# Optimization experiments

Hardware: AMD Instinct MI355X
Metric: run time of the kernel (lower is better)

## Reference

```python
import jax, jax.numpy as jnp
import numpy as np

STRIDE = 1
PADDING = 1
DILATION = 1


def setup_inputs() -> dict:
    key = jax.random.key(0)
    k1, k2 = jax.random.split(key)
    N, C_in, H, W = 32, 128, 56, 56
    C_out, ksz = 256, 3
    x = jax.random.normal(k1, (N, C_in, H, W), dtype=jnp.float32)
    # xavier_normal_ with gain sqrt(2): std = gain*sqrt(2/(fan_in+fan_out))
    fan_in = C_in * ksz * ksz
    fan_out = C_out * ksz * ksz
    std = np.sqrt(2.0) * np.sqrt(2.0 / (fan_in + fan_out))
    weight = jax.random.normal(k2, (C_out, C_in, ksz, ksz), dtype=jnp.float32) * jnp.float32(std)
    bias = jnp.zeros((C_out,), dtype=jnp.float32)
    return {"x": x, "weight": weight, "bias": bias}


def reference(x, weight, bias):
    # Faithful to conv2d(X, K, stride, padding, dilation, bias):
    # unfold (im2col) + matmul + fold is mathematically a standard cross-correlation
    # conv; expressed here with the efficient lax primitive.
    y = jax.lax.conv_general_dilated(
        x, weight,
        window_strides=(STRIDE, STRIDE),
        padding=[(PADDING, PADDING), (PADDING, PADDING)],
        rhs_dilation=(DILATION, DILATION),
        dimension_numbers=("NCHW", "OIHW", "NCHW"),
    )
    return y + bias[None, :, None, None]
```

## Files before the change

kernel.cpp:

```cpp
#include <hip/hip_runtime.h>
#include <hip/hip_bf16.h>


#define CIN   128
#define HH    56
#define WW    56
#define COUT  256
#define HW    3136
#define NIMG  32
#define NP    (NIMG * HW)
#define XPW   58
#define XPIX  (XPW * XPW)
#define XPAD_BYTES (NIMG * XPIX * CIN * 2)
#define WT_OFF     XPAD_BYTES

typedef __bf16 bf16x8 __attribute__((ext_vector_type(8)));
typedef float  f32x4  __attribute__((ext_vector_type(4)));

#define GLD16(g, l) __builtin_amdgcn_global_load_lds( \
    (const __attribute__((address_space(1))) void*)(g), \
    (__attribute__((address_space(3))) void*)(l), 16, 0, 0)

__global__ __launch_bounds__(128) void prep_x(const float* __restrict__ x,
                                              __hip_bfloat16* __restrict__ xp) {
    const int b = blockIdx.x;
    const int n = b / HH;
    const int y = b - n * HH;
    const int ci = threadIdx.x;
    const float* src = x + ((size_t)(n * CIN + ci) * HW) + y * WW;
    __hip_bfloat16* dst = xp + ((size_t)(n * XPIX + (y + 1) * XPW + 1)) * CIN + ci;
    for (int xx = 0; xx < WW; ++xx)
        dst[(size_t)xx * CIN] = __float2bfloat16(src[xx]);
}

__global__ __launch_bounds__(256) void prep_w(const float* __restrict__ w,
                                              __hip_bfloat16* __restrict__ wt) {
    const int co = blockIdx.x * 2 + (threadIdx.x >> 7);
    const int ci = threadIdx.x & 127;
    const float* src = w + (size_t)(co * CIN + ci) * 9;
    #pragma unroll
    for (int t = 0; t < 9; ++t)
        wt[(size_t)t * (COUT * CIN) + co * CIN + ci] = __float2bfloat16(src[t]);
}

__global__ __launch_bounds__(256) void conv_main(
    const char* __restrict__ xpb,
    const char* __restrict__ wtb,
    const float* __restrict__ bias,
    float* __restrict__ out)
{
    __shared__ __align__(16) char Alds[16384];
    __shared__ __align__(16) char Blds[16384];

    const int tid  = threadIdx.x;
    const int l    = tid & 63;
    const int wv   = tid >> 6;
    const int wm   = wv & 1;
    const int wn   = wv >> 1;
    const int l15  = l & 15;
    const int quad = l >> 4;
    const int lr   = l >> 3;
    const int ls   = l & 7;
    const int sg   = ls ^ lr;

    const int bm = blockIdx.x & 1;
    const int bn = blockIdx.x >> 1;
    const int pbase  = bn * 128;
    const int cobase = bm * 128;

    unsigned aoff[4], boff[4];
    #pragma unroll
    for (int j = 0; j < 4; ++j) {
        const int rowl = (wv * 4 + j) * 8 + lr;
        aoff[j] = (unsigned)((cobase + rowl) * 256 + sg * 16);
        const int p   = pbase + rowl;
        const int n   = p / HW;
        const int rem = p - n * HW;
        const int y   = rem / WW;
        const int x   = rem - y * WW;
        boff[j] = (unsigned)((n * XPIX + y * XPW + x) * 256 + sg * 16);
    }

    f32x4 acc[4][4];
    #pragma unroll
    for (int i = 0; i < 4; ++i)
        #pragma unroll
        for (int j = 0; j < 4; ++j)
            acc[i][j] = (f32x4){0.f, 0.f, 0.f, 0.f};

    #pragma unroll
    for (int t = 0; t < 9; ++t) {
        const int r = t / 3;
        const int s = t - 3 * r;
        #pragma unroll
        for (int hf = 0; hf < 2; ++hf) {
            const unsigned wo = (unsigned)(t * 65536 + hf * 128);
            const unsigned bo = (unsigned)((r * XPW + s) * 256 + hf * 128);

            __syncthreads();
            #pragma unroll
            for (int j = 0; j < 4; ++j) {
                GLD16(wtb + wo + aoff[j], Alds + (wv * 4 + j) * 1024);
                GLD16(xpb + bo + boff[j], Blds + (wv * 4 + j) * 1024);
            }
            __syncthreads();

            #pragma unroll
            for (int kg = 0; kg < 2; ++kg) {
                bf16x8 af[4], bfr[4];
                #pragma unroll
                for (int mt = 0; mt < 4; ++mt) {
                    const int row  = wm * 64 + mt * 16 + l15;
                    const int segl = (kg * 4 + quad) ^ (row & 7);
                    af[mt] = *(const bf16x8*)(Alds + row * 128 + segl * 16);
                }
                #pragma unroll
                for (int nt = 0; nt < 4; ++nt) {
                    const int row  = wn * 64 + nt * 16 + l15;
                    const int segl = (kg * 4 + quad) ^ (row & 7);
                    bfr[nt] = *(const bf16x8*)(Blds + row * 128 + segl * 16);
                }
                #pragma unroll
                for (int mt = 0; mt < 4; ++mt)
                    #pragma unroll
                    for (int nt = 0; nt < 4; ++nt)
                        acc[mt][nt] = __builtin_amdgcn_mfma_f32_16x16x32_bf16(
                            af[mt], bfr[nt], acc[mt][nt], 0, 0, 0);
            }
        }
    }

    #pragma unroll
    for (int nt = 0; nt < 4; ++nt) {
        const int pp = pbase + wn * 64 + nt * 16 + l15;
        const int n2 = pp / HW;
        const int r2 = pp - n2 * HW;
        float* ob = out + (size_t)n2 * (COUT * HW) + r2;
        #pragma unroll
        for (int mt = 0; mt < 4; ++mt) {
            const int co = cobase + wm * 64 + mt * 16 + quad * 4;
            const float4 bv = *(const float4*)(bias + co);
            f32x4 a = acc[mt][nt];
            ob[(size_t)(co + 0) * HW] = a[0] + bv.x;
            ob[(size_t)(co + 1) * HW] = a[1] + bv.y;
            ob[(size_t)(co + 2) * HW] = a[2] + bv.z;
            ob[(size_t)(co + 3) * HW] = a[3] + bv.w;
        }
    }
}

extern "C" void kernel_launch(void* const* d_in, const int* in_sizes, int n_in,
                              void* d_out, int out_size, void* d_ws, size_t ws_size,
                              hipStream_t stream) {
    const float* x = (const float*)d_in[0];
    const float* w = (const float*)d_in[1];
    const float* b = (const float*)d_in[2];
    char* ws = (char*)d_ws;
    __hip_bfloat16* xp = (__hip_bfloat16*)ws;
    __hip_bfloat16* wt = (__hip_bfloat16*)(ws + WT_OFF);

    hipMemsetAsync(ws, 0, XPAD_BYTES, stream);
    prep_x<<<dim3(NIMG * HH), dim3(128), 0, stream>>>(x, xp);
    prep_w<<<dim3(128), dim3(256), 0, stream>>>(w, wt);
    conv_main<<<dim3((NP / 128) * 2), dim3(256), 0, stream>>>(
        (const char*)xp, (const char*)wt, b, (float*)d_out);
}
```

Before: 215.1 us.

## Coalesce input prep via LDS transpose, drop memset, use full-K tiles per tap

prep_x now reads rows with float4 loads, transposes them through LDS and writes coalesced 16-byte stores, and zeroes only the padding border itself, which removes the full-buffer memset. Rounding changes from round-to-nearest to truncation. The conv kernel loads the whole 128-channel K slice per tap in one stage, halving the barriers, with a 16-segment XOR swizzle. Blocks are reordered so groups of 8 pixel tiles share an output-channel half, which may help L2 reuse. LDS use doubles to 64KB, which may cut occupancy.

```diff
diff --git a/kernel.cpp b/kernel.cpp
--- a/kernel.cpp
+++ b/kernel.cpp
@@ -21,16 +21,48 @@
     (const __attribute__((address_space(1))) void*)(g), \
     (__attribute__((address_space(3))) void*)(l), 16, 0, 0)
 
+__device__ __forceinline__ unsigned pack_bf16(float a, float b) {
+    return (__float_as_uint(b) & 0xFFFF0000u) | (__float_as_uint(a) >> 16);
+}
+
 __global__ __launch_bounds__(128) void prep_x(const float* __restrict__ x,
                                               __hip_bfloat16* __restrict__ xp) {
-    const int b = blockIdx.x;
-    const int n = b / HH;
-    const int y = b - n * HH;
+    __shared__ unsigned short t[HH * CIN];
+    const int b  = blockIdx.x;
+    const int n  = b / HH;
+    const int y  = b - n * HH;
     const int ci = threadIdx.x;
+
     const float* src = x + ((size_t)(n * CIN + ci) * HW) + y * WW;
-    __hip_bfloat16* dst = xp + ((size_t)(n * XPIX + (y + 1) * XPW + 1)) * CIN + ci;
-    for (int xx = 0; xx < WW; ++xx)
-        dst[(size_t)xx * CIN] = __float2bfloat16(src[xx]);
+    #pragma unroll
+    for (int j = 0; j < 14; ++j) {
+        const float4 v = ((const float4*)src)[j];
+        t[(4 * j + 0) * CIN + ci] = (unsigned short)(__float_as_uint(v.x) >> 16);
+        t[(4 * j + 1) * CIN + ci] = (unsigned short)(__float_as_uint(v.y) >> 16);
+        t[(4 * j + 2) * CIN + ci] = (unsigned short)(__float_as_uint(v.z) >> 16);
+        t[(4 * j + 3) * CIN + ci] = (unsigned short)(__float_as_uint(v.w) >> 16);
+    }
+
+    const uint4 z = make_uint4(0, 0, 0, 0);
+    if (ci < 32) {
+        const int side = ci >> 4;
+        const int j    = ci & 15;
+        ((uint4*)(xp + ((size_t)n * XPIX + (y + 1) * XPW + side * 57) * CIN))[j] = z;
+    }
+    if (y == 0)
+        for (int j = ci; j < 928; j += 128)
+            ((uint4*)(xp + (size_t)n * XPIX * CIN))[j] = z;
+    if (y == HH - 1)
+        for (int j = ci; j < 928; j += 128)
+            ((uint4*)(xp + ((size_t)n * XPIX + 57 * XPW) * CIN))[j] = z;
+
+    __syncthreads();
+
+    uint4* dst = (uint4*)(xp + ((size_t)n * XPIX + (y + 1) * XPW + 1) * CIN);
+    const uint4* lsrc = (const uint4*)t;
+    #pragma unroll
+    for (int j = 0; j < 7; ++j)
+        dst[j * 128 + ci] = lsrc[j * 128 + ci];
 }
 
 __global__ __launch_bounds__(256) void prep_w(const float* __restrict__ w,
@@ -39,8 +71,8 @@
     const int ci = threadIdx.x & 127;
     const float* src = w + (size_t)(co * CIN + ci) * 9;
     #pragma unroll
-    for (int t = 0; t < 9; ++t)
-        wt[(size_t)t * (COUT * CIN) + co * CIN + ci] = __float2bfloat16(src[t]);
+    for (int tp = 0; tp < 9; ++tp)
+        wt[(size_t)tp * (COUT * CIN) + co * CIN + ci] = __float2bfloat16(src[tp]);
 }
 
 __global__ __launch_bounds__(256) void conv_main(
@@ -49,8 +81,8 @@
     const float* __restrict__ bias,
     float* __restrict__ out)
 {
-    __shared__ __align__(16) char Alds[16384];
-    __shared__ __align__(16) char Blds[16384];
+    __shared__ __align__(16) char Alds[32768];
+    __shared__ __align__(16) char Blds[32768];
 
     const int tid  = threadIdx.x;
     const int l    = tid & 63;
@@ -59,26 +91,26 @@
     const int wn   = wv >> 1;
     const int l15  = l & 15;
     const int quad = l >> 4;
-    const int lr   = l >> 3;
-    const int ls   = l & 7;
-    const int sg   = ls ^ lr;
 
-    const int bm = blockIdx.x & 1;
-    const int bn = blockIdx.x >> 1;
+    const int idx = blockIdx.x;
+    const int bm  = (idx >> 3) & 1;
+    const int bn  = (idx >> 4) * 8 + (idx & 7);
     const int pbase  = bn * 128;
     const int cobase = bm * 128;
 
-    unsigned aoff[4], boff[4];
+    unsigned aoff[8], boff[8];
     #pragma unroll
-    for (int j = 0; j < 4; ++j) {
-        const int rowl = (wv * 4 + j) * 8 + lr;
-        aoff[j] = (unsigned)((cobase + rowl) * 256 + sg * 16);
-        const int p   = pbase + rowl;
+    for (int j = 0; j < 8; ++j) {
+        const int c    = wv * 8 + j;
+        const int row  = 4 * c + (l >> 4);
+        const int gseg = (l & 15) ^ (row & 15);
+        aoff[j] = (unsigned)((cobase + row) * 256 + gseg * 16);
+        const int p   = pbase + row;
         const int n   = p / HW;
         const int rem = p - n * HW;
         const int y   = rem / WW;
         const int x   = rem - y * WW;
-        boff[j] = (unsigned)((n * XPIX + y * XPW + x) * 256 + sg * 16);
+        boff[j] = (unsigned)((n * XPIX + y * XPW + x) * 256 + gseg * 16);
     }
 
     f32x4 acc[4][4];
@@ -92,41 +124,39 @@
     for (int t = 0; t < 9; ++t) {
         const int r = t / 3;
         const int s = t - 3 * r;
+        const unsigned wo = (unsigned)(t * (COUT * CIN * 2));
+        const unsigned bo = (unsigned)((r * XPW + s) * 256);
+
+        __syncthreads();
         #pragma unroll
-        for (int hf = 0; hf < 2; ++hf) {
-            const unsigned wo = (unsigned)(t * 65536 + hf * 128);
-            const unsigned bo = (unsigned)((r * XPW + s) * 256 + hf * 128);
+        for (int j = 0; j < 8; ++j) {
+            const int c = wv * 8 + j;
+            GLD16(wtb + wo + aoff[j], Alds + c * 1024);
+            GLD16(xpb + bo + boff[j], Blds + c * 1024);
+        }
+        __syncthreads();
 
-            __syncthreads();
+        #pragma unroll
+        for (int kg = 0; kg < 4; ++kg) {
+            bf16x8 af[4], bfr[4];
             #pragma unroll
-            for (int j = 0; j < 4; ++j) {
-                GLD16(wtb + wo + aoff[j], Alds + (wv * 4 + j) * 1024);
-                GLD16(xpb + bo + boff[j], Blds + (wv * 4 + j) * 1024);
+            for (int mt = 0; mt < 4; ++mt) {
+                const int row  = wm * 64 + mt * 16 + l15;
+                const int segl = (kg * 4 + quad) ^ l15;
+                af[mt] = *(const bf16x8*)(Alds + row * 256 + segl * 16);
             }
-            __syncthreads();
-
             #pragma unroll
-            for (int kg = 0; kg < 2; ++kg) {
-                bf16x8 af[4], bfr[4];
+            for (int nt = 0; nt < 4; ++nt) {
+                const int row  = wn * 64 + nt * 16 + l15;
+                const int segl = (kg * 4 + quad) ^ l15;
+                bfr[nt] = *(const bf16x8*)(Blds + row * 256 + segl * 16);
+            }
+            #pragma unroll
+            for (int mt = 0; mt < 4; ++mt)
                 #pragma unroll
-                for (int mt = 0; mt < 4; ++mt) {
-                    const int row  = wm * 64 + mt * 16 + l15;
-                    const int segl = (kg * 4 + quad) ^ (row & 7);
-                    af[mt] = *(const bf16x8*)(Alds + row * 128 + segl * 16);
-                }
-                #pragma unroll
-                for (int nt = 0; nt < 4; ++nt) {
-                    const int row  = wn * 64 + nt * 16 + l15;
-                    const int segl = (kg * 4 + quad) ^ (row & 7);
-                    bfr[nt] = *(const bf16x8*)(Blds + row * 128 + segl * 16);
-                }
-                #pragma unroll
-                for (int mt = 0; mt < 4; ++mt)
-                    #pragma unroll
-                    for (int nt = 0; nt < 4; ++nt)
-                        acc[mt][nt] = __builtin_amdgcn_mfma_f32_16x16x32_bf16(
-                            af[mt], bfr[nt], acc[mt][nt], 0, 0, 0);
-            }
+                for (int nt = 0; nt < 4; ++nt)
+                    acc[mt][nt] = __builtin_amdgcn_mfma_f32_16x16x32_bf16(
+                        af[mt], bfr[nt], acc[mt][nt], 0, 0, 0);
         }
     }
 
@@ -159,7 +189,6 @@
     __hip_bfloat16* xp = (__hip_bfloat16*)ws;
     __hip_bfloat16* wt = (__hip_bfloat16*)(ws + WT_OFF);
 
-    hipMemsetAsync(ws, 0, XPAD_BYTES, stream);
     prep_x<<<dim3(NIMG * HH), dim3(128), 0, stream>>>(x, xp);
     prep_w<<<dim3(128), dim3(256), 0, stream>>>(w, wt);
     conv_main<<<dim3((NP / 128) * 2), dim3(256), 0, stream>>>(
```

After: 212.9 us. About the same (-1.0%).
